# Optimization experiments

Hardware: AMD Instinct MI355X
Metric: run time of the kernel (lower is better)

The kernel has to match this reference:

```python
import jax, jax.numpy as jnp
import numpy as np

N, F, H, O = 3072, 128, 16, 8  # nodes, in_channels, hidden_channels, out_channels


def setup_inputs() -> dict:
    key = jax.random.key(0)
    ks = jax.random.split(key, 8)
    s = 0.01  # xavier gain=0.01 in original init -> small weights
    return {
        "x": jax.random.normal(ks[0], (N, F), dtype=jnp.float32),
        "edge_index": jax.random.randint(ks[1], (2, N * 32), 0, N, dtype=jnp.int64),
        "node_distances": jax.random.uniform(ks[2], (N, N), dtype=jnp.float32),
        "normalization_matrix": jnp.ones((N, N), dtype=jnp.float32),
        # per-feature MLPs fs[f]: Linear(1,H) -> ReLU -> (Dropout p=0) -> Linear(H,O), stacked over F
        "W1": s * jax.random.normal(ks[3], (F, H), dtype=jnp.float32),
        "b1": jnp.zeros((F, H), dtype=jnp.float32),
        "W2": s * jax.random.normal(ks[4], (F, H, O), dtype=jnp.float32),
        "b2": jnp.zeros((F, O), dtype=jnp.float32),
        # rho MLP: Linear(1,H) -> ReLU -> Linear(H,O) (bias=True since is_graph_task=False)
        "rW1": s * jax.random.normal(ks[5], (H,), dtype=jnp.float32),
        "rb1": jnp.zeros((H,), dtype=jnp.float32),
        "rW2": s * jax.random.normal(ks[6], (H, O), dtype=jnp.float32),
        "rb2": jnp.zeros((O,), dtype=jnp.float32),
    }


def reference(x, edge_index, node_distances, normalization_matrix,
              W1, b1, W2, b2, rW1, rb1, rW2, rb2):
    # --- per-feature tiny MLPs, vectorized over the feature axis ---
    # h[n,f,:] = relu(x[n,f] * W1[f] + b1[f])
    h = jax.nn.relu(x[:, :, None] * W1[None, :, :] + b1[None, :, :])  # [N,F,H]
    fx = jnp.einsum('nfh,fho->nfo', h, W2) + b2[None, :, :]           # [N,F,O]
    # sum over features first (commutes with the matmul's F-reduction)
    g = fx.sum(axis=1)                                                 # [N,O]

    # --- rho MLP on normalized pairwise distances ---
    d = node_distances / normalization_matrix                          # [N,N]
    hd = jax.nn.relu(d[:, :, None] * rW1 + rb1)                        # [N,N,H]
    m = jnp.einsum('nmh,ho->nmo', hd, rW2) + rb2                       # [N,N,O]

    # out.T in torch: mf = m_dist_perm @ fx_perm summed over features -> [N,O]
    out = jnp.einsum('nmo,mo->no', m, g)                               # [N,O]
    return out
```

## Files before the change

### kernel.cpp

```cpp
#include <hip/hip_runtime.h>
#include <hip/hip_bf16.h>
#include <math.h>

#define NN 3072
#define FF 128
#define HH 16
#define OO 8

#define NPB 4

__global__ __launch_bounds__(128) void gnan_g_kernel(
    const float* __restrict__ x,
    const float* __restrict__ W1,
    const float* __restrict__ b1,
    const float* __restrict__ W2,
    const float* __restrict__ b2,
    float* __restrict__ gT)
{
    const int f  = threadIdx.x;
    const int n0 = blockIdx.x * NPB;

    float w1[HH], bb1[HH], w2[HH][OO], bb2[OO];
#pragma unroll
    for (int h = 0; h < HH; ++h) {
        w1[h]  = W1[f * HH + h];
        bb1[h] = b1[f * HH + h];
    }
#pragma unroll
    for (int h = 0; h < HH; ++h)
#pragma unroll
        for (int o = 0; o < OO; ++o)
            w2[h][o] = W2[(f * HH + h) * OO + o];
#pragma unroll
    for (int o = 0; o < OO; ++o) bb2[o] = b2[f * OO + o];

    __shared__ float wsum[2][OO];

    for (int ni = 0; ni < NPB; ++ni) {
        const int n = n0 + ni;
        const float xv = x[(size_t)n * FF + f];

        float v[OO];
#pragma unroll
        for (int o = 0; o < OO; ++o) v[o] = bb2[o];
#pragma unroll
        for (int h = 0; h < HH; ++h) {
            float a = fmaxf(xv * w1[h] + bb1[h], 0.f);
#pragma unroll
            for (int o = 0; o < OO; ++o) v[o] += a * w2[h][o];
        }

#pragma unroll
        for (int o = 0; o < OO; ++o) {
#pragma unroll
            for (int off = 32; off > 0; off >>= 1)
                v[o] += __shfl_down(v[o], off);
        }
        const int lane = threadIdx.x & 63;
        const int wid  = threadIdx.x >> 6;
        if (lane == 0) {
#pragma unroll
            for (int o = 0; o < OO; ++o) wsum[wid][o] = v[o];
        }
        __syncthreads();
        if (threadIdx.x < OO) {
            gT[threadIdx.x * NN + n] = wsum[0][threadIdx.x] + wsum[1][threadIdx.x];
        }
        __syncthreads();
    }
}

__global__ __launch_bounds__(768) void gnan_main_kernel(
    const float* __restrict__ nd,
    const float* __restrict__ nm,
    const float* __restrict__ gT,
    const float* __restrict__ rW1,
    const float* __restrict__ rb1,
    const float* __restrict__ rW2,
    const float* __restrict__ rb2,
    float* __restrict__ out)
{
    __shared__ float gs[OO * NN];
    __shared__ float Kp[HH + 2];
    __shared__ float rowsA[HH + 1][16];
    __shared__ float sk[HH];
    __shared__ int   shh[HH];
    __shared__ float cAdd[OO];

    const int t = threadIdx.x;

    if (t == 0) {
        for (int h = 0; h < HH; ++h) {
            float w = rW1[h];
            sk[h]  = (w != 0.0f) ? (-rb1[h] / w) : INFINITY;
            shh[h] = h;
        }
        for (int i = 1; i < HH; ++i) {
            float kv = sk[i]; int iv = shh[i];
            int p = i - 1;
            while (p >= 0 && sk[p] > kv) { sk[p+1]=sk[p]; shh[p+1]=shh[p]; --p; }
            sk[p+1] = kv; shh[p+1] = iv;
        }
        Kp[0] = -INFINITY;
        for (int h = 0; h < HH; ++h) Kp[h + 1] = sk[h];
        Kp[HH + 1] = INFINITY;
    }
    if (t < OO) {
        float c = rb2[t];
        for (int h = 0; h < HH; ++h)
            if (rW1[h] == 0.0f) c += fmaxf(rb1[h], 0.f) * rW2[h * OO + t];
        cAdd[t] = c;
    }
    __syncthreads();
    if (t < (HH + 1) * OO) {
        const int j = t >> 3, o = t & 7;
        float alpha = 0.f, beta = 0.f;
        for (int p = 0; p < HH; ++p) {
            const int h = shh[p];
            const float w = rW1[h];
            const bool active = (w > 0.f) ? (p < j) : (w < 0.f ? (p >= j) : false);
            if (active) {
                alpha += w       * rW2[h * OO + o];
                beta  += rb1[h]  * rW2[h * OO + o];
            }
        }
        rowsA[j][o]     = alpha;
        rowsA[j][8 + o] = beta + cAdd[o];
    }

    {
        float4*       dst = reinterpret_cast<float4*>(gs);
        const float4* src = reinterpret_cast<const float4*>(gT);
        for (int i = t; i < OO * NN / 4; i += 768) dst[i] = src[i];
    }
    __syncthreads();

    const int wave = t >> 6;
    const int lane = t & 63;
    const int row  = blockIdx.x * 12 + wave;

    const float* __restrict__ drow = nd + (size_t)row * NN;
    const float* __restrict__ nrow = nm + (size_t)row * NN;

    float CA[OO], CB[OO];
    float clo = INFINITY, chi = -INFINITY;
#pragma unroll
    for (int o = 0; o < OO; ++o) { CA[o] = 0.f; CB[o] = 0.f; }

    float acc[OO];
#pragma unroll
    for (int o = 0; o < OO; ++o) acc[o] = 0.f;

    for (int it = 0; it < NN / 128; ++it) {
        const int m0 = it * 128 + lane * 2;
        const float2 dv2 = *reinterpret_cast<const float2*>(drow + m0);
        const float2 nv2 = *reinterpret_cast<const float2*>(nrow + m0);

        float2 gv[OO];
#pragma unroll
        for (int o = 0; o < OO; ++o)
            gv[o] = *reinterpret_cast<const float2*>(&gs[o * NN + m0]);

#pragma unroll
        for (int k = 0; k < 2; ++k) {
            const float d = __fdividef(k == 0 ? dv2.x : dv2.y,
                                       k == 0 ? nv2.x : nv2.y);
            if (d < clo || d >= chi) {
                int j = 0;
#pragma unroll
                for (int p = 0; p < HH; ++p) j += (d >= Kp[p + 1]) ? 1 : 0;
                clo = Kp[j];
                chi = Kp[j + 1];
                const float4 a0 = *reinterpret_cast<const float4*>(&rowsA[j][0]);
                const float4 a1 = *reinterpret_cast<const float4*>(&rowsA[j][4]);
                const float4 b0 = *reinterpret_cast<const float4*>(&rowsA[j][8]);
                const float4 b1 = *reinterpret_cast<const float4*>(&rowsA[j][12]);
                CA[0]=a0.x; CA[1]=a0.y; CA[2]=a0.z; CA[3]=a0.w;
                CA[4]=a1.x; CA[5]=a1.y; CA[6]=a1.z; CA[7]=a1.w;
                CB[0]=b0.x; CB[1]=b0.y; CB[2]=b0.z; CB[3]=b0.w;
                CB[4]=b1.x; CB[5]=b1.y; CB[6]=b1.z; CB[7]=b1.w;
            }
#pragma unroll
            for (int o = 0; o < OO; ++o) {
                const float g = (k == 0) ? gv[o].x : gv[o].y;
                acc[o] = fmaf(fmaf(CA[o], d, CB[o]), g, acc[o]);
            }
        }
    }

#pragma unroll
    for (int o = 0; o < OO; ++o) {
#pragma unroll
        for (int off = 32; off > 0; off >>= 1)
            acc[o] += __shfl_down(acc[o], off);
    }
    if (lane == 0) {
#pragma unroll
        for (int o = 0; o < OO; ++o)
            out[(size_t)row * OO + o] = acc[o];
    }
}

extern "C" void kernel_launch(void* const* d_in, const int* in_sizes, int n_in,
                              void* d_out, int out_size, void* d_ws, size_t ws_size,
                              hipStream_t stream) {
    const float* x   = (const float*)d_in[0];
    const float* nd  = (const float*)d_in[2];
    const float* nm  = (const float*)d_in[3];
    const float* W1  = (const float*)d_in[4];
    const float* b1  = (const float*)d_in[5];
    const float* W2  = (const float*)d_in[6];
    const float* b2  = (const float*)d_in[7];
    const float* rW1 = (const float*)d_in[8];
    const float* rb1 = (const float*)d_in[9];
    const float* rW2 = (const float*)d_in[10];
    const float* rb2 = (const float*)d_in[11];
    float* out = (float*)d_out;

    float* gT = (float*)d_ws;

    gnan_g_kernel<<<NN / NPB, 128, 0, stream>>>(x, W1, b1, W2, b2, gT);
    gnan_main_kernel<<<NN / 12, 768, 0, stream>>>(nd, nm, gT, rW1, rb1, rW2, rb2, out);
}
```

Measured before the change: 152.6 us.

## Split columns into chunks with atomics and fast path for common interval

The main kernel now splits each row's column range into three chunks handled by separate blocks with a smaller shared g slice, and accumulates partial results into the output with atomics after a memset. A new single-block setup kernel precomputes breakpoints, piecewise-linear coefficients, a reference interval taken from the first distance value, and per-chunk sums of g. For the common interval the loop only accumulates d*g, with the bias handled through the precomputed g sums, and a correction term covers values in other intervals. The g kernel is also restructured to load weights once per h and process all nodes together. This adds two launches, a serial setup block and atomics, and the fast path pays off only when most distances share the reference interval.

```diff
diff --git a/kernel.cpp b/kernel.cpp
--- a/kernel.cpp
+++ b/kernel.cpp
@@ -6,6 +6,16 @@
 #define FF 128
 #define HH 16
 #define OO 8
+
+#define MC   1024
+#define NCH  3
+#define RPB  8
+
+#define OFF_GT   0
+#define OFF_KP   24576
+#define OFF_ROWS 24600
+#define OFF_REF  24872
+#define OFF_BG   24890
 
 #define NPB 4
 
@@ -20,78 +30,84 @@
     const int f  = threadIdx.x;
     const int n0 = blockIdx.x * NPB;
 
-    float w1[HH], bb1[HH], w2[HH][OO], bb2[OO];
-#pragma unroll
+    float xv[NPB];
+#pragma unroll
+    for (int ni = 0; ni < NPB; ++ni)
+        xv[ni] = x[(size_t)(n0 + ni) * FF + f];
+
+    const float4 b2a = *reinterpret_cast<const float4*>(b2 + f * OO);
+    const float4 b2b = *reinterpret_cast<const float4*>(b2 + f * OO + 4);
+
+    float acc[NPB][OO];
+#pragma unroll
+    for (int ni = 0; ni < NPB; ++ni) {
+        acc[ni][0] = b2a.x; acc[ni][1] = b2a.y; acc[ni][2] = b2a.z; acc[ni][3] = b2a.w;
+        acc[ni][4] = b2b.x; acc[ni][5] = b2b.y; acc[ni][6] = b2b.z; acc[ni][7] = b2b.w;
+    }
+
     for (int h = 0; h < HH; ++h) {
-        w1[h]  = W1[f * HH + h];
-        bb1[h] = b1[f * HH + h];
-    }
-#pragma unroll
-    for (int h = 0; h < HH; ++h)
-#pragma unroll
-        for (int o = 0; o < OO; ++o)
-            w2[h][o] = W2[(f * HH + h) * OO + o];
-#pragma unroll
-    for (int o = 0; o < OO; ++o) bb2[o] = b2[f * OO + o];
+        const float w1h = W1[f * HH + h];
+        const float b1h = b1[f * HH + h];
+        const float4 wa = *reinterpret_cast<const float4*>(W2 + (size_t)(f * HH + h) * OO);
+        const float4 wb = *reinterpret_cast<const float4*>(W2 + (size_t)(f * HH + h) * OO + 4);
+#pragma unroll
+        for (int ni = 0; ni < NPB; ++ni) {
+            const float a = fmaxf(fmaf(xv[ni], w1h, b1h), 0.f);
+            acc[ni][0] = fmaf(a, wa.x, acc[ni][0]);
+            acc[ni][1] = fmaf(a, wa.y, acc[ni][1]);
+            acc[ni][2] = fmaf(a, wa.z, acc[ni][2]);
+            acc[ni][3] = fmaf(a, wa.w, acc[ni][3]);
+            acc[ni][4] = fmaf(a, wb.x, acc[ni][4]);
+            acc[ni][5] = fmaf(a, wb.y, acc[ni][5]);
+            acc[ni][6] = fmaf(a, wb.z, acc[ni][6]);
+            acc[ni][7] = fmaf(a, wb.w, acc[ni][7]);
+        }
+    }
 
     __shared__ float wsum[2][OO];
-
+    const int lane = threadIdx.x & 63;
+    const int wid  = threadIdx.x >> 6;
+#pragma unroll
     for (int ni = 0; ni < NPB; ++ni) {
-        const int n = n0 + ni;
-        const float xv = x[(size_t)n * FF + f];
-
-        float v[OO];
-#pragma unroll
-        for (int o = 0; o < OO; ++o) v[o] = bb2[o];
-#pragma unroll
-        for (int h = 0; h < HH; ++h) {
-            float a = fmaxf(xv * w1[h] + bb1[h], 0.f);
-#pragma unroll
-            for (int o = 0; o < OO; ++o) v[o] += a * w2[h][o];
-        }
-
 #pragma unroll
         for (int o = 0; o < OO; ++o) {
 #pragma unroll
             for (int off = 32; off > 0; off >>= 1)
-                v[o] += __shfl_down(v[o], off);
-        }
-        const int lane = threadIdx.x & 63;
-        const int wid  = threadIdx.x >> 6;
+                acc[ni][o] += __shfl_down(acc[ni][o], off);
+        }
         if (lane == 0) {
 #pragma unroll
-            for (int o = 0; o < OO; ++o) wsum[wid][o] = v[o];
-        }
-        __syncthreads();
-        if (threadIdx.x < OO) {
-            gT[threadIdx.x * NN + n] = wsum[0][threadIdx.x] + wsum[1][threadIdx.x];
-        }
-        __syncthreads();
-    }
-}
-
-__global__ __launch_bounds__(768) void gnan_main_kernel(
+            for (int o = 0; o < OO; ++o) wsum[wid][o] = acc[ni][o];
+        }
+        __syncthreads();
+        if (threadIdx.x < OO)
+            gT[threadIdx.x * NN + (n0 + ni)] = wsum[0][threadIdx.x] + wsum[1][threadIdx.x];
+        __syncthreads();
+    }
+}
+
+__global__ __launch_bounds__(256) void gnan_setup_kernel(
     const float* __restrict__ nd,
     const float* __restrict__ nm,
-    const float* __restrict__ gT,
     const float* __restrict__ rW1,
     const float* __restrict__ rb1,
     const float* __restrict__ rW2,
     const float* __restrict__ rb2,
-    float* __restrict__ out)
+    float* __restrict__ wsf)
 {
-    __shared__ float gs[OO * NN];
-    __shared__ float Kp[HH + 2];
-    __shared__ float rowsA[HH + 1][16];
     __shared__ float sk[HH];
     __shared__ int   shh[HH];
-    __shared__ float cAdd[OO];
+    __shared__ float sKp[HH + 2];
+    __shared__ float scAdd[OO];
+    __shared__ float srows[HH + 1][16];
+    __shared__ float sref[18];
+    __shared__ float sred[8];
 
     const int t = threadIdx.x;
 
     if (t == 0) {
         for (int h = 0; h < HH; ++h) {
-            float w = rW1[h];
+            const float w = rW1[h];
             sk[h]  = (w != 0.0f) ? (-rb1[h] / w) : INFINITY;
             shh[h] = h;
         }
@@ -101,17 +117,18 @@
             while (p >= 0 && sk[p] > kv) { sk[p+1]=sk[p]; shh[p+1]=shh[p]; --p; }
             sk[p+1] = kv; shh[p+1] = iv;
         }
-        Kp[0] = -INFINITY;
-        for (int h = 0; h < HH; ++h) Kp[h + 1] = sk[h];
-        Kp[HH + 1] = INFINITY;
+        sKp[0] = -INFINITY;
+        for (int h = 0; h < HH; ++h) sKp[h + 1] = sk[h];
+        sKp[HH + 1] = INFINITY;
     }
     if (t < OO) {
         float c = rb2[t];
         for (int h = 0; h < HH; ++h)
             if (rW1[h] == 0.0f) c += fmaxf(rb1[h], 0.f) * rW2[h * OO + t];
-        cAdd[t] = c;
-    }
-    __syncthreads();
+        scAdd[t] = c;
+    }
+    __syncthreads();
+
     if (t < (HH + 1) * OO) {
         const int j = t >> 3, o = t & 7;
         float alpha = 0.f, beta = 0.f;
@@ -120,84 +137,137 @@
             const float w = rW1[h];
             const bool active = (w > 0.f) ? (p < j) : (w < 0.f ? (p >= j) : false);
             if (active) {
-                alpha += w       * rW2[h * OO + o];
-                beta  += rb1[h]  * rW2[h * OO + o];
+                alpha += w      * rW2[h * OO + o];
+                beta  += rb1[h] * rW2[h * OO + o];
             }
         }
-        rowsA[j][o]     = alpha;
-        rowsA[j][8 + o] = beta + cAdd[o];
-    }
+        srows[j][o]     = alpha;
+        srows[j][8 + o] = beta + scAdd[o];
+        wsf[OFF_ROWS + j * 16 + o]     = srows[j][o];
+        wsf[OFF_ROWS + j * 16 + 8 + o] = srows[j][8 + o];
+    }
+    if (t < HH + 2) wsf[OFF_KP + t] = sKp[t];
+    __syncthreads();
+
+    if (t == 0) {
+        const float d00 = nd[0] / nm[0];
+        int j = 0;
+        for (int p = 0; p < HH; ++p) j += (d00 >= sKp[p + 1]) ? 1 : 0;
+        sref[0] = sKp[j];
+        sref[1] = sKp[j + 1];
+        for (int o = 0; o < OO; ++o) {
+            sref[2 + o]  = srows[j][o];
+            sref[10 + o] = srows[j][8 + o];
+        }
+        for (int i = 0; i < 18; ++i) wsf[OFF_REF + i] = sref[i];
+    }
+    __syncthreads();
+
+    const int lane = t & 63;
+    const int wave = t >> 6;
+    for (int p = 0; p < NCH * OO; ++p) {
+        const int c = p >> 3, o = p & 7;
+        float s = 0.f;
+        for (int i = t; i < MC; i += 256)
+            s += wsf[OFF_GT + o * NN + c * MC + i];
+#pragma unroll
+        for (int off = 32; off > 0; off >>= 1)
+            s += __shfl_down(s, off);
+        if (lane == 0) sred[wave] = s;
+        __syncthreads();
+        if (t == 0)
+            wsf[OFF_BG + p] = sref[10 + o] * (sred[0] + sred[1] + sred[2] + sred[3]);
+        __syncthreads();
+    }
+}
+
+__global__ __launch_bounds__(512) void gnan_main_kernel(
+    const float* __restrict__ nd,
+    const float* __restrict__ nm,
+    const float* __restrict__ wsf,
+    float* __restrict__ out)
+{
+    __shared__ float gs[OO * MC];
+
+    const int t  = threadIdx.x;
+    const int b  = blockIdx.x;
+    const int rg = b / NCH;
+    const int c  = b % NCH;
 
     {
         float4*       dst = reinterpret_cast<float4*>(gs);
-        const float4* src = reinterpret_cast<const float4*>(gT);
-        for (int i = t; i < OO * NN / 4; i += 768) dst[i] = src[i];
-    }
+        const float4* src = reinterpret_cast<const float4*>(wsf + OFF_GT);
+        for (int i = t; i < OO * MC / 4; i += 512) {
+            const int o  = i >> 8;
+            const int mi = i & 255;
+            dst[i] = src[o * (NN / 4) + c * (MC / 4) + mi];
+        }
+    }
+    const float clo = wsf[OFF_REF + 0];
+    const float chi = wsf[OFF_REF + 1];
     __syncthreads();
 
     const int wave = t >> 6;
     const int lane = t & 63;
-    const int row  = blockIdx.x * 12 + wave;
-
-    const float* __restrict__ drow = nd + (size_t)row * NN;
-    const float* __restrict__ nrow = nm + (size_t)row * NN;
-
-    float CA[OO], CB[OO];
-    float clo = INFINITY, chi = -INFINITY;
-#pragma unroll
-    for (int o = 0; o < OO; ++o) { CA[o] = 0.f; CB[o] = 0.f; }
-
-    float acc[OO];
-#pragma unroll
-    for (int o = 0; o < OO; ++o) acc[o] = 0.f;
-
-    for (int it = 0; it < NN / 128; ++it) {
+    const int row  = rg * RPB + wave;
+
+    const float* __restrict__ drow = nd + (size_t)row * NN + c * MC;
+    const float* __restrict__ nrow = nm + (size_t)row * NN + c * MC;
+
+    float dg[OO], corr[OO];
+#pragma unroll
+    for (int o = 0; o < OO; ++o) { dg[o] = 0.f; corr[o] = 0.f; }
+
+    for (int it = 0; it < MC / 128; ++it) {
         const int m0 = it * 128 + lane * 2;
-        const float2 dv2 = *reinterpret_cast<const float2*>(drow + m0);
-        const float2 nv2 = *reinterpret_cast<const float2*>(nrow + m0);
-
+        const float2 dv = *reinterpret_cast<const float2*>(drow + m0);
+        const float2 nv = *reinterpret_cast<const float2*>(nrow + m0);
         float2 gv[OO];
 #pragma unroll
         for (int o = 0; o < OO; ++o)
-            gv[o] = *reinterpret_cast<const float2*>(&gs[o * NN + m0]);
+            gv[o] = *reinterpret_cast<const float2*>(&gs[o * MC + m0]);
 
 #pragma unroll
         for (int k = 0; k < 2; ++k) {
-            const float d = __fdividef(k == 0 ? dv2.x : dv2.y,
-                                       k == 0 ? nv2.x : nv2.y);
-            if (d < clo || d >= chi) {
+            const float d = __fdividef(k == 0 ? dv.x : dv.y,
+                                       k == 0 ? nv.x : nv.y);
+            if (d >= clo && d < chi) {
+#pragma unroll
+                for (int o = 0; o < OO; ++o) {
+                    const float g = (k == 0) ? gv[o].x : gv[o].y;
+                    dg[o] = fmaf(d, g, dg[o]);
+                }
+            } else {
                 int j = 0;
 #pragma unroll
-                for (int p = 0; p < HH; ++p) j += (d >= Kp[p + 1]) ? 1 : 0;
-                clo = Kp[j];
-                chi = Kp[j + 1];
-                const float4 a0 = *reinterpret_cast<const float4*>(&rowsA[j][0]);
-                const float4 a1 = *reinterpret_cast<const float4*>(&rowsA[j][4]);
-                const float4 b0 = *reinterpret_cast<const float4*>(&rowsA[j][8]);
-                const float4 b1 = *reinterpret_cast<const float4*>(&rowsA[j][12]);
-                CA[0]=a0.x; CA[1]=a0.y; CA[2]=a0.z; CA[3]=a0.w;
-                CA[4]=a1.x; CA[5]=a1.y; CA[6]=a1.z; CA[7]=a1.w;
-                CB[0]=b0.x; CB[1]=b0.y; CB[2]=b0.z; CB[3]=b0.w;
-                CB[4]=b1.x; CB[5]=b1.y; CB[6]=b1.z; CB[7]=b1.w;
+                for (int p = 0; p < HH; ++p)
+                    j += (d >= wsf[OFF_KP + 1 + p]) ? 1 : 0;
+#pragma unroll
+                for (int o = 0; o < OO; ++o) {
+                    const float a  = wsf[OFF_ROWS + j * 16 + o];
+                    const float bb = wsf[OFF_ROWS + j * 16 + 8 + o];
+                    const float g  = (k == 0) ? gv[o].x : gv[o].y;
+                    const float v  = fmaf(a, d, bb) - wsf[OFF_REF + 10 + o];
+                    corr[o] = fmaf(v, g, corr[o]);
+                }
             }
-#pragma unroll
-            for (int o = 0; o < OO; ++o) {
-                const float g = (k == 0) ? gv[o].x : gv[o].y;
-                acc[o] = fmaf(fmaf(CA[o], d, CB[o]), g, acc[o]);
-            }
-        }
-    }
-
+        }
+    }
+
+    float val[OO];
+#pragma unroll
+    for (int o = 0; o < OO; ++o)
+        val[o] = fmaf(wsf[OFF_REF + 2 + o], dg[o], corr[o]);
 #pragma unroll
     for (int o = 0; o < OO; ++o) {
 #pragma unroll
         for (int off = 32; off > 0; off >>= 1)
-            acc[o] += __shfl_down(acc[o], off);
+            val[o] += __shfl_down(val[o], off);
     }
     if (lane == 0) {
 #pragma unroll
         for (int o = 0; o < OO; ++o)
-            out[(size_t)row * OO + o] = acc[o];
+            atomicAdd(out + (size_t)row * OO + o, val[o] + wsf[OFF_BG + c * OO + o]);
     }
 }
 
@@ -216,9 +286,10 @@
     const float* rW2 = (const float*)d_in[10];
     const float* rb2 = (const float*)d_in[11];
     float* out = (float*)d_out;
-
-    float* gT = (float*)d_ws;
-
-    gnan_g_kernel<<<NN / NPB, 128, 0, stream>>>(x, W1, b1, W2, b2, gT);
-    gnan_main_kernel<<<NN / 12, 768, 0, stream>>>(nd, nm, gT, rW1, rb1, rW2, rb2, out);
-}
+    float* wsf = (float*)d_ws;
+
+    gnan_g_kernel<<<NN / NPB, 128, 0, stream>>>(x, W1, b1, W2, b2, wsf + OFF_GT);
+    gnan_setup_kernel<<<1, 256, 0, stream>>>(nd, nm, rW1, rb1, rW2, rb2, wsf);
+    hipMemsetAsync(out, 0, (size_t)out_size * sizeof(float), stream);
+    gnan_main_kernel<<<(NN / RPB) * NCH, 512, 0, stream>>>(nd, nm, wsf, out);
+}
```

Result: slower. 180.8 us (+18.5%).
